# Kernel optimization log

Measured on AMD Instinct MI355X. Metric: run time of the kernel, lower is better.

The kernel has to match this reference:

```python
import jax, jax.numpy as jnp
import numpy as np
from jax import lax

B, C, T = 8, 512, 2048
TEMP = 0.07
EPS = 1e-12


def setup_inputs() -> dict:
    key = jax.random.key(0)
    k1, k2, k3, k4 = jax.random.split(key, 4)
    x = jax.random.normal(k1, (B, C, T), dtype=jnp.float32)
    w_qkv = jax.random.normal(k2, (3 * C, C, 1), dtype=jnp.float32) * (1.0 / np.sqrt(C))
    w_dw = jax.random.normal(k3, (3 * C, 1, 3), dtype=jnp.float32) * (1.0 / np.sqrt(3))
    w_proj = jax.random.normal(k4, (C, C, 1), dtype=jnp.float32) * (1.0 / np.sqrt(C))
    return {"x": x, "w_qkv": w_qkv, "w_dw": w_dw, "w_proj": w_proj}


def _l2norm_ch(a):
    # F.normalize(a, dim=1): divide by L2 norm over channel dim, clamped at eps
    n = jnp.sqrt(jnp.sum(a * a, axis=1, keepdims=True))
    return a / jnp.maximum(n, EPS)


def reference(x, w_qkv, w_dw, w_proj):
    # 1x1 conv: [B,C,T] x [3C,C] -> [B,3C,T]
    qkv = jnp.einsum('bct,oc->bot', x, w_qkv[:, :, 0])
    # depthwise conv, kernel 3, padding 1, groups = 3C
    qkv = lax.conv_general_dilated(
        qkv, w_dw, window_strides=(1,), padding=[(1, 1)],
        dimension_numbers=('NCH', 'OIH', 'NCH'), feature_group_count=3 * C)
    q, k, v = jnp.split(qkv, 3, axis=1)  # each [B,C,T]
    q = _l2norm_ch(q)
    k = _l2norm_ch(k)
    # attn over tokens: [B,T,T]
    attn = jax.nn.softmax(jnp.einsum('bct,bcs->bts', q, k) / TEMP, axis=-1)
    out = jnp.einsum('bts,bcs->bct', attn, v)  # [B,C,T]
    return jnp.einsum('bct,oc->bot', out, w_proj[:, :, 0])
```

## Files before the change

kernel.cpp:

```cpp
#include <hip/hip_runtime.h>
#include <math.h>

static constexpr int B_ = 8, C_ = 512, T_ = 2048, C3_ = 1536;
static constexpr float INV_TEMP = 1.0f / 0.07f;

typedef __attribute__((ext_vector_type(8))) short short8;
typedef __attribute__((ext_vector_type(4))) float floatx4;

__device__ __forceinline__ float b2f(unsigned short u) {
  union { unsigned int i; float f; } v; v.i = ((unsigned int)u) << 16; return v.f;
}
__device__ __forceinline__ unsigned short f2b(float f) {
  union { float f; unsigned int i; } v; v.f = f;
  const unsigned int x = v.i;
  return (unsigned short)((x + 0x7FFFu + ((x >> 16) & 1u)) >> 16);
}
__device__ __forceinline__ void gld16(const unsigned short* g, unsigned short* l) {
  __builtin_amdgcn_global_load_lds(
      (const __attribute__((address_space(1))) void*)g,
      (__attribute__((address_space(3))) void*)l, 16, 0, 0);
}

template<bool OUT_BF16, int MODE, int MAP = 0>
__global__ __launch_bounds__(256)
void gemm_tn(const unsigned short* __restrict__ A, const unsigned short* __restrict__ B,
             void* __restrict__ Cout, int K, int lda, int ldb, int ldc,
             long long sA, long long sB, long long sC,
             const float* __restrict__ rs, const float* __restrict__ cs,
             float* __restrict__ denom, int rcStride, float scale)
{
  constexpr int NL = 4;

  int bz, m0, n0;
  if (MAP == 2) {
    const int id = blockIdx.x;
    bz = id & 7;
    const int r = id >> 3;
    m0 = (r >> 2) * 128; n0 = (r & 3) * 128;
  } else {
    bz = blockIdx.z;
    m0 = blockIdx.y * 128; n0 = blockIdx.x * 128;
  }
  A += (long long)bz * sA;
  B += (long long)bz * sB;
  if (MODE == 2) { rs += (long long)bz * rcStride; cs += (long long)bz * rcStride;
                   denom += (long long)bz * rcStride; }
  if (MODE == 3) { rs += (long long)bz * rcStride; }
  const int tid = threadIdx.x;
  const int w = tid >> 6, lane = tid & 63;
  const int wm = (w >> 1) * 64, wn = (w & 1) * 64;
  const int rl = lane & 15, qd = lane >> 4;

  __shared__ __align__(16) unsigned short As[3][128 * 32];
  __shared__ __align__(16) unsigned short Bs[3][128 * 32];

  const int sr = lane >> 2, sg = lane & 3;
  const int ml0 = 32 * w + sr, ml1 = ml0 + 16;
  const int q0 = sg ^ ((ml0 >> 1) & 3), q1 = sg ^ ((ml1 >> 1) & 3);
  const unsigned short* gA0 = A + (long long)(m0 + ml0) * lda + q0 * 8;
  const unsigned short* gA1 = A + (long long)(m0 + ml1) * lda + q1 * 8;
  const unsigned short* gB0 = B + (long long)(n0 + ml0) * ldb + q0 * 8;
  const unsigned short* gB1 = B + (long long)(n0 + ml1) * ldb + q1 * 8;

  int aoff[4], boff[4];
  #pragma unroll
  for (int i = 0; i < 4; ++i) {
    const int mr = wm + i * 16 + rl;
    aoff[i] = mr * 32 + ((qd ^ ((mr >> 1) & 3)) * 8);
    const int nr = wn + i * 16 + rl;
    boff[i] = nr * 32 + ((qd ^ ((nr >> 1) & 3)) * 8);
  }

  floatx4 acc[4][4];
  #pragma unroll
  for (int i = 0; i < 4; ++i)
    #pragma unroll
    for (int j = 0; j < 4; ++j) acc[i][j] = 0.0f;

  auto stage = [&](int t, int bf) {
    const int ko = t * 32;
    gld16(gA0 + ko, As[bf] + (32 * w) * 32);
    gld16(gA1 + ko, As[bf] + (32 * w + 16) * 32);
    gld16(gB0 + ko, Bs[bf] + (32 * w) * 32);
    gld16(gB1 + ko, Bs[bf] + (32 * w + 16) * 32);
  };
  auto compute = [&](int bf) {
    short8 fa[4], fb[4];
    #pragma unroll
    for (int i = 0; i < 4; ++i) fa[i] = *(const short8*)(As[bf] + aoff[i]);
    #pragma unroll
    for (int j = 0; j < 4; ++j) fb[j] = *(const short8*)(Bs[bf] + boff[j]);
    #pragma unroll
    for (int i = 0; i < 4; ++i)
      #pragma unroll
      for (int j = 0; j < 4; ++j)
        acc[i][j] = __builtin_amdgcn_mfma_f32_16x16x32_bf16(fa[i], fb[j], acc[i][j], 0, 0, 0);
  };

  const int niter = K >> 5;
  stage(0, 0);
  stage(1, 1);
  int buf = 0;
  for (int i = 0; i < niter - 1; ++i) {
    asm volatile("s_waitcnt vmcnt(%0)\n\ts_barrier" :: "i"(NL) : "memory");
    if (i + 2 < niter) {
      int nb = buf + 2; if (nb >= 3) nb -= 3;
      stage(i + 2, nb);
    }
    compute(buf);
    if (++buf == 3) buf = 0;
  }
  asm volatile("s_waitcnt vmcnt(0)\n\ts_barrier" ::: "memory");
  compute(buf);

  #pragma unroll
  for (int i = 0; i < 4; ++i) {
    #pragma unroll
    for (int r = 0; r < 4; ++r) {
      const int row = m0 + wm + i * 16 + qd * 4 + r;
      float rowf = 0.f;
      if (MODE == 2) rowf = rs[row] * scale;
      if (MODE == 3) rowf = 1.0f / rs[row];
      float rsum = 0.f;
      #pragma unroll
      for (int j = 0; j < 4; ++j) {
        const int col = n0 + wn + j * 16 + rl;
        float v = acc[i][j][r];
        if (MODE == 2) {
          const float s = v * rowf * cs[col];
          const unsigned short pb = f2b(__expf(s - scale));
          rsum += b2f(pb);
          ((unsigned short*)Cout)[(long long)bz * sC + (long long)row * ldc + col] = pb;
          continue;
        }
        if (MODE == 3) v *= rowf;
        const long long idx = (long long)bz * sC + (long long)row * ldc + col;
        if (OUT_BF16) ((unsigned short*)Cout)[idx] = f2b(v);
        else          ((float*)Cout)[idx] = v;
      }
      if (MODE == 2) {
        #pragma unroll
        for (int m = 1; m < 16; m <<= 1) rsum += __shfl_xor(rsum, m);
        if (rl == 0) atomicAdd(denom + row, rsum);
      }
    }
  }
}

__global__ __launch_bounds__(512)
void gemm_attn8(const unsigned short* __restrict__ A, const unsigned short* __restrict__ B,
                unsigned short* __restrict__ Cout, int K, int lda, int ldb, int ldc,
                long long sA, long long sB, long long sC,
                const float* __restrict__ rs, const float* __restrict__ cs,
                float* __restrict__ denom, int rcStride, float scale)
{
  extern __shared__ unsigned short S[];

  const int id = blockIdx.x;
  const int bz = id & 7;
  const int r = id >> 3;
  const int m0 = (r >> 3) * 128, n0 = (r & 7) * 256;
  A += (long long)bz * sA;
  B += (long long)bz * sB;
  rs += (long long)bz * rcStride; cs += (long long)bz * rcStride;
  denom += (long long)bz * rcStride;
  const int tid = threadIdx.x;
  const int w = tid >> 6, lane = tid & 63;
  const int wm = (w >> 2) * 64, wn = (w & 3) * 64;
  const int rl = lane & 15, qd = lane >> 4;

  const int srw = tid >> 2, sg = tid & 3;
  const int qa  = sg ^ ((srw >> 1) & 3);
  const int brw1 = 128 + srw;
  const int qb1 = sg ^ ((brw1 >> 1) & 3);
  const unsigned short* gA  = A + (long long)(m0 + srw) * lda + qa * 8;
  const unsigned short* gB0 = B + (long long)(n0 + srw) * ldb + qa * 8;
  const unsigned short* gB1 = B + (long long)(n0 + brw1) * ldb + qb1 * 8;
  unsigned short* dA  = S + srw * 32 + sg * 8;
  unsigned short* dB0 = S + 12288 + srw * 32 + sg * 8;
  unsigned short* dB1 = S + 12288 + brw1 * 32 + sg * 8;

  int aoff[4], boff[4];
  #pragma unroll
  for (int i = 0; i < 4; ++i) {
    const int mr = wm + i * 16 + rl;
    aoff[i] = mr * 32 + ((qd ^ ((mr >> 1) & 3)) * 8);
    const int nr = wn + i * 16 + rl;
    boff[i] = 12288 + nr * 32 + ((qd ^ ((nr >> 1) & 3)) * 8);
  }

  floatx4 acc[4][4];
  #pragma unroll
  for (int i = 0; i < 4; ++i)
    #pragma unroll
    for (int j = 0; j < 4; ++j) acc[i][j] = 0.0f;

  auto stage = [&](int t, int bf) {
    const int ko = t * 32;
    gld16(gA + ko,  dA  + bf * 4096);
    gld16(gB0 + ko, dB0 + bf * 8192);
    gld16(gB1 + ko, dB1 + bf * 8192);
  };
  auto compute = [&](int bf) {
    short8 fa[4], fb[4];
    const unsigned short* pA = S + bf * 4096;
    const unsigned short* pB = S + bf * 8192;
    #pragma unroll
    for (int i = 0; i < 4; ++i) fa[i] = *(const short8*)(pA + aoff[i]);
    #pragma unroll
    for (int j = 0; j < 4; ++j) fb[j] = *(const short8*)(pB + boff[j]);
    #pragma unroll
    for (int i = 0; i < 4; ++i)
      #pragma unroll
      for (int j = 0; j < 4; ++j)
        acc[i][j] = __builtin_amdgcn_mfma_f32_16x16x32_bf16(fa[i], fb[j], acc[i][j], 0, 0, 0);
  };

  const int niter = K >> 5;
  stage(0, 0);
  stage(1, 1);
  int buf = 0;
  for (int i = 0; i < niter - 1; ++i) {
    asm volatile("s_waitcnt vmcnt(3)\n\ts_barrier" ::: "memory");
    if (i + 2 < niter) {
      int nb = buf + 2; if (nb >= 3) nb -= 3;
      stage(i + 2, nb);
    }
    compute(buf);
    if (++buf == 3) buf = 0;
  }
  asm volatile("s_waitcnt vmcnt(0)\n\ts_barrier" ::: "memory");
  compute(buf);

  float cf4[4];
  #pragma unroll
  for (int j = 0; j < 4; ++j) cf4[j] = cs[n0 + wn + j * 16 + rl];
  #pragma unroll
  for (int i = 0; i < 4; ++i) {
    #pragma unroll
    for (int rr = 0; rr < 4; ++rr) {
      const int row = m0 + wm + i * 16 + qd * 4 + rr;
      const float rowf = rs[row] * scale;
      float rsum = 0.f;
      #pragma unroll
      for (int j = 0; j < 4; ++j) {
        const int col = n0 + wn + j * 16 + rl;
        const float s = acc[i][j][rr] * rowf * cf4[j];
        const unsigned short pb = f2b(__expf(s - scale));
        rsum += b2f(pb);
        Cout[(long long)bz * sC + (long long)row * ldc + col] = pb;
      }
      #pragma unroll
      for (int m = 1; m < 16; m <<= 1) rsum += __shfl_xor(rsum, m);
      if (rl == 0) atomicAdd(denom + row, rsum);
    }
  }
}

__global__ __launch_bounds__(256)
void zero_f(float* __restrict__ p, int n)
{
  const int i = blockIdx.x * 256 + threadIdx.x;
  if (i < n) p[i] = 0.f;
}

__global__ __launch_bounds__(256)
void fin_inv(float* __restrict__ p, int n)
{
  const int i = blockIdx.x * 256 + threadIdx.x;
  if (i < n) p[i] = 1.f / fmaxf(sqrtf(p[i]), 1e-12f);
}

__global__ __launch_bounds__(256)
void conv_xT(const float* __restrict__ x, unsigned short* __restrict__ xT)
{
  const int b = blockIdx.z, t0 = blockIdx.x * 64, c0 = blockIdx.y * 64;
  const int tid = threadIdx.x;
  __shared__ float tile[64][65];
  const float* src = x + (long long)b * C_ * T_;
  const int cy = tid >> 2, g = tid & 3;
  const float* sp = src + (long long)(c0 + cy) * T_ + t0 + 16 * g;
  #pragma unroll
  for (int i = 0; i < 4; ++i) {
    const float4 v = *(const float4*)(sp + 4 * i);
    tile[cy][16 * g + 4 * i + 0] = v.x;
    tile[cy][16 * g + 4 * i + 1] = v.y;
    tile[cy][16 * g + 4 * i + 2] = v.z;
    tile[cy][16 * g + 4 * i + 3] = v.w;
  }
  __syncthreads();
  const int tl = tid >> 2, cg = tid & 3;
  short8 o0, o1;
  #pragma unroll
  for (int i = 0; i < 8; ++i) {
    o0[i] = (short)f2b(tile[16 * cg + i][tl]);
    o1[i] = (short)f2b(tile[16 * cg + 8 + i][tl]);
  }
  unsigned short* dst = xT + (long long)b * T_ * C_ + (long long)(t0 + tl) * C_ + c0 + 16 * cg;
  *(short8*)dst = o0;
  *(short8*)(dst + 8) = o1;
}

__global__ __launch_bounds__(256)
void conv_bf(const float* __restrict__ in, unsigned short* __restrict__ out, int n)
{
  const int i = blockIdx.x * 256 + threadIdx.x;
  if (i < n) out[i] = f2b(in[i]);
}

__global__ __launch_bounds__(256)
void dw_qkv_v2(const unsigned short* __restrict__ qkv, const float* __restrict__ wdw,
               unsigned short* __restrict__ qT, unsigned short* __restrict__ kT,
               unsigned short* __restrict__ vout,
               float* __restrict__ sq_q, float* __restrict__ sq_k)
{
  const int bz = blockIdx.z, b = bz / 3, p = bz % 3;
  const int t0 = blockIdx.x * 64, c0 = blockIdx.y * 64;
  const int tid = threadIdx.x;
  __shared__ unsigned short tin[64][80];
  __shared__ float tout[64][65];
  const int chb = b * C3_ + p * C_;

  #pragma unroll
  for (int s = 0; s < 2; ++s) {
    const int idx = tid + s * 256;
    const int cy = idx >> 3, g = idx & 7;
    *(short8*)&tin[cy][8 + 8 * g] =
        *(const short8*)(qkv + (long long)(chb + c0 + cy) * T_ + t0 + 8 * g);
  }
  if (tid < 64) {
    tin[tid][7] = (t0 > 0) ? qkv[(long long)(chb + c0 + tid) * T_ + t0 - 1]
                           : (unsigned short)0;
  } else if (tid < 128) {
    const int cy = tid - 64;
    tin[cy][72] = (t0 + 64 < T_) ? qkv[(long long)(chb + c0 + cy) * T_ + t0 + 64]
                                 : (unsigned short)0;
  }
  __syncthreads();

  const int cy = tid >> 2, tg = tid & 3;
  const float* wp = wdw + (p * C_ + c0 + cy) * 3;
  const float w0 = wp[0], w1 = wp[1], w2 = wp[2];

  if (p == 2) {
    short8 o0, o1;
    #pragma unroll
    for (int i = 0; i < 16; ++i) {
      const int j = 16 * tg + i;
      const float v = fmaf(w0, b2f(tin[cy][7 + j]),
                      fmaf(w1, b2f(tin[cy][8 + j]), w2 * b2f(tin[cy][9 + j])));
      if (i < 8) o0[i] = (short)f2b(v); else o1[i - 8] = (short)f2b(v);
    }
    unsigned short* d = vout + (long long)(b * C_ + c0 + cy) * T_ + t0 + 16 * tg;
    *(short8*)d = o0;
    *(short8*)(d + 8) = o1;
    return;
  }

  #pragma unroll
  for (int i = 0; i < 16; ++i) {
    const int j = 16 * tg + i;
    tout[j][cy] = fmaf(w0, b2f(tin[cy][7 + j]),
                  fmaf(w1, b2f(tin[cy][8 + j]), w2 * b2f(tin[cy][9 + j])));
  }
  __syncthreads();

  unsigned short* dst = (p == 0 ? qT : kT) + (long long)b * T_ * C_;
  float* sq = (p == 0 ? sq_q : sq_k) + (long long)b * T_;
  #pragma unroll
  for (int s = 0; s < 2; ++s) {
    const int idx = tid + s * 256;
    const int tl = idx >> 3, cl = idx & 7;
    short8 o;
    float ssq = 0.f;
    #pragma unroll
    for (int i = 0; i < 8; ++i) {
      const unsigned short ub = f2b(tout[tl][8 * cl + i]);
      o[i] = (short)ub;
      const float fv = b2f(ub);
      ssq = fmaf(fv, fv, ssq);
    }
    *(short8*)(dst + (long long)(t0 + tl) * C_ + c0 + 8 * cl) = o;
    #pragma unroll
    for (int m = 1; m < 8; m <<= 1) ssq += __shfl_xor(ssq, m);
    if (cl == 0) atomicAdd(sq + t0 + tl, ssq);
  }
}

extern "C" void kernel_launch(void* const* d_in, const int* in_sizes, int n_in,
                              void* d_out, int out_size, void* d_ws, size_t ws_size,
                              hipStream_t stream)
{
  const float* x      = (const float*)d_in[0];
  const float* w_qkv  = (const float*)d_in[1];
  const float* w_dw   = (const float*)d_in[2];
  const float* w_proj = (const float*)d_in[3];
  float* out = (float*)d_out;

  static int attr_done = 0;
  if (!attr_done) {
    hipFuncSetAttribute((const void*)&gemm_attn8,
                        hipFuncAttributeMaxDynamicSharedMemorySize, 73728);
    attr_done = 1;
  }

  char* base = (char*)d_ws;
  unsigned short* xT      = (unsigned short*)base;
  unsigned short* wqkv_bf = (unsigned short*)(base + 16777216);
  unsigned short* av_t    = (unsigned short*)base;
  char* p = base + 67108864;
  unsigned short* qT = (unsigned short*)p; p += 16777216;
  unsigned short* kT = (unsigned short*)p; p += 16777216;
  unsigned short* vb = (unsigned short*)p; p += 16777216;
  unsigned short* attn   = (unsigned short*)p;
  unsigned short* qkv_bf = (unsigned short*)p;
  p += 67108864;
  unsigned short* wproj_bf = (unsigned short*)p; p += 524288;
  float* inv_nq = (float*)p; p += 65536;
  float* inv_nk = (float*)p; p += 65536;
  float* denom  = (float*)p;

  const long long TC = (long long)T_ * C_, TT = (long long)T_ * T_;

  conv_xT<<<dim3(T_ / 64, C_ / 64, B_), 256, 0, stream>>>(x, xT);
  conv_bf<<<(C3_ * C_) / 256, 256, 0, stream>>>(w_qkv, wqkv_bf, C3_ * C_);
  conv_bf<<<(C_ * C_) / 256, 256, 0, stream>>>(w_proj, wproj_bf, C_ * C_);
  zero_f<<<(3 * B_ * T_) / 256, 256, 0, stream>>>(inv_nq, 3 * B_ * T_);

  gemm_tn<true, 0><<<dim3(16, 12, B_), 256, 0, stream>>>(
      wqkv_bf, xT, qkv_bf, C_, C_, C_, T_,
      0LL, TC, (long long)C3_ * T_, nullptr, nullptr, nullptr, 0, 1.f);

  dw_qkv_v2<<<dim3(T_ / 64, C_ / 64, B_ * 3), 256, 0, stream>>>(
      qkv_bf, w_dw, qT, kT, vb, inv_nq, inv_nk);
  fin_inv<<<(2 * B_ * T_) / 256, 256, 0, stream>>>(inv_nq, 2 * B_ * T_);

  gemm_attn8<<<dim3(128 * B_, 1, 1), 512, 73728, stream>>>(
      qT, kT, attn, C_, C_, C_, T_,
      TC, TC, TT, inv_nq, inv_nk, denom, T_, INV_TEMP);

  gemm_tn<true, 3, 2><<<dim3(64 * B_, 1, 1), 256, 0, stream>>>(
      attn, vb, av_t, T_, T_, T_, C_,
      TT, (long long)C_ * T_, TC, denom, nullptr, nullptr, T_, 1.f);

  gemm_tn<false, 0><<<dim3(16, 4, B_), 256, 0, stream>>>(
      wproj_bf, av_t, out, C_, C_, C_, T_,
      0LL, TC, (long long)C_ * T_, nullptr, nullptr, nullptr, 0, 1.f);
}
```

Before: 275.8 us.

## Enlarge QK^T attention GEMM tile to 256x256 with 4x8 MFMA per-wave tiles

The attention score GEMM now uses 256x256 output tiles instead of 128x256. Each of the 8 waves computes a 64x128 sub-tile with a 4x8 accumulator array, and the global-to-LDS staging is reorganised into four 16-byte loads per thread. Grid size is halved, and LDS per block grows to 96 KB across three buffers. The aim is more reuse per LDS fragment load and less global traffic for A and B, at the cost of higher register pressure (128 accumulator floats per thread) and fewer blocks to fill the CUs.

```diff
diff --git a/kernel.cpp b/kernel.cpp
--- a/kernel.cpp
+++ b/kernel.cpp
@@ -147,72 +147,73 @@
   }
 }
 
-__global__ __launch_bounds__(512)
-void gemm_attn8(const unsigned short* __restrict__ A, const unsigned short* __restrict__ B,
-                unsigned short* __restrict__ Cout, int K, int lda, int ldb, int ldc,
-                long long sA, long long sB, long long sC,
-                const float* __restrict__ rs, const float* __restrict__ cs,
-                float* __restrict__ denom, int rcStride, float scale)
+__global__ __launch_bounds__(512, 2)
+void gemm_attn512(const unsigned short* __restrict__ A, const unsigned short* __restrict__ B,
+                  unsigned short* __restrict__ Cout, int K, int lda, int ldb, int ldc,
+                  long long sA, long long sB, long long sC,
+                  const float* __restrict__ rs, const float* __restrict__ cs,
+                  float* __restrict__ denom, int rcStride, float scale)
 {
   extern __shared__ unsigned short S[];
 
   const int id = blockIdx.x;
   const int bz = id & 7;
   const int r = id >> 3;
-  const int m0 = (r >> 3) * 128, n0 = (r & 7) * 256;
+  const int m0 = (r >> 3) * 256, n0 = (r & 7) * 256;
   A += (long long)bz * sA;
   B += (long long)bz * sB;
   rs += (long long)bz * rcStride; cs += (long long)bz * rcStride;
   denom += (long long)bz * rcStride;
+
   const int tid = threadIdx.x;
   const int w = tid >> 6, lane = tid & 63;
-  const int wm = (w >> 2) * 64, wn = (w & 3) * 64;
+  const int wm = (w >> 1) * 64, wn = (w & 1) * 128;
   const int rl = lane & 15, qd = lane >> 4;
 
-  const int srw = tid >> 2, sg = tid & 3;
-  const int qa  = sg ^ ((srw >> 1) & 3);
-  const int brw1 = 128 + srw;
-  const int qb1 = sg ^ ((brw1 >> 1) & 3);
-  const unsigned short* gA  = A + (long long)(m0 + srw) * lda + qa * 8;
-  const unsigned short* gB0 = B + (long long)(n0 + srw) * ldb + qa * 8;
-  const unsigned short* gB1 = B + (long long)(n0 + brw1) * ldb + qb1 * 8;
-  unsigned short* dA  = S + srw * 32 + sg * 8;
-  unsigned short* dB0 = S + 12288 + srw * 32 + sg * 8;
-  unsigned short* dB1 = S + 12288 + brw1 * 32 + sg * 8;
-
-  int aoff[4], boff[4];
+  const int srow = w * 16 + (lane >> 2), sg = lane & 3;
+  const int qa = sg ^ ((srow >> 1) & 3);
+  const unsigned short* gA0 = A + (long long)(m0 + srow) * lda + qa * 8;
+  const unsigned short* gA1 = gA0 + (long long)128 * lda;
+  const unsigned short* gB0 = B + (long long)(n0 + srow) * ldb + qa * 8;
+  const unsigned short* gB1 = gB0 + (long long)128 * ldb;
+
+  int aoff[4], boff[8];
   #pragma unroll
   for (int i = 0; i < 4; ++i) {
-    const int mr = wm + i * 16 + rl;
-    aoff[i] = mr * 32 + ((qd ^ ((mr >> 1) & 3)) * 8);
-    const int nr = wn + i * 16 + rl;
-    boff[i] = 12288 + nr * 32 + ((qd ^ ((nr >> 1) & 3)) * 8);
-  }
-
-  floatx4 acc[4][4];
+    const int ar = wm + i * 16 + rl;
+    aoff[i] = ar * 32 + ((qd ^ ((ar >> 1) & 3)) * 8);
+  }
+  #pragma unroll
+  for (int j = 0; j < 8; ++j) {
+    const int br = wn + j * 16 + rl;
+    boff[j] = 8192 + br * 32 + ((qd ^ ((br >> 1) & 3)) * 8);
+  }
+
+  floatx4 acc[4][8];
   #pragma unroll
   for (int i = 0; i < 4; ++i)
     #pragma unroll
-    for (int j = 0; j < 4; ++j) acc[i][j] = 0.0f;
+    for (int j = 0; j < 8; ++j) acc[i][j] = 0.0f;
 
   auto stage = [&](int t, int bf) {
     const int ko = t * 32;
-    gld16(gA + ko,  dA  + bf * 4096);
-    gld16(gB0 + ko, dB0 + bf * 8192);
-    gld16(gB1 + ko, dB1 + bf * 8192);
+    unsigned short* base = S + bf * 16384;
+    gld16(gA0 + ko, base + w * 512);
+    gld16(gA1 + ko, base + 4096 + w * 512);
+    gld16(gB0 + ko, base + 8192 + w * 512);
+    gld16(gB1 + ko, base + 12288 + w * 512);
   };
   auto compute = [&](int bf) {
-    short8 fa[4], fb[4];
-    const unsigned short* pA = S + bf * 4096;
-    const unsigned short* pB = S + bf * 8192;
-    #pragma unroll
-    for (int i = 0; i < 4; ++i) fa[i] = *(const short8*)(pA + aoff[i]);
-    #pragma unroll
-    for (int j = 0; j < 4; ++j) fb[j] = *(const short8*)(pB + boff[j]);
+    short8 fa[4], fb[8];
+    const unsigned short* base = S + bf * 16384;
+    #pragma unroll
+    for (int i = 0; i < 4; ++i) fa[i] = *(const short8*)(base + aoff[i]);
+    #pragma unroll
+    for (int j = 0; j < 8; ++j) fb[j] = *(const short8*)(base + boff[j]);
     #pragma unroll
     for (int i = 0; i < 4; ++i)
       #pragma unroll
-      for (int j = 0; j < 4; ++j)
+      for (int j = 0; j < 8; ++j)
         acc[i][j] = __builtin_amdgcn_mfma_f32_16x16x32_bf16(fa[i], fb[j], acc[i][j], 0, 0, 0);
   };
 
@@ -221,7 +222,7 @@
   stage(1, 1);
   int buf = 0;
   for (int i = 0; i < niter - 1; ++i) {
-    asm volatile("s_waitcnt vmcnt(3)\n\ts_barrier" ::: "memory");
+    asm volatile("s_waitcnt vmcnt(4)\n\ts_barrier" ::: "memory");
     if (i + 2 < niter) {
       int nb = buf + 2; if (nb >= 3) nb -= 3;
       stage(i + 2, nb);
@@ -232,9 +233,9 @@
   asm volatile("s_waitcnt vmcnt(0)\n\ts_barrier" ::: "memory");
   compute(buf);
 
-  float cf4[4];
-  #pragma unroll
-  for (int j = 0; j < 4; ++j) cf4[j] = cs[n0 + wn + j * 16 + rl];
+  float cf[8];
+  #pragma unroll
+  for (int j = 0; j < 8; ++j) cf[j] = cs[n0 + wn + j * 16 + rl];
   #pragma unroll
   for (int i = 0; i < 4; ++i) {
     #pragma unroll
@@ -243,9 +244,9 @@
       const float rowf = rs[row] * scale;
       float rsum = 0.f;
       #pragma unroll
-      for (int j = 0; j < 4; ++j) {
+      for (int j = 0; j < 8; ++j) {
         const int col = n0 + wn + j * 16 + rl;
-        const float s = acc[i][j][rr] * rowf * cf4[j];
+        const float s = acc[i][j][rr] * rowf * cf[j];
         const unsigned short pb = f2b(__expf(s - scale));
         rsum += b2f(pb);
         Cout[(long long)bz * sC + (long long)row * ldc + col] = pb;
@@ -399,8 +400,8 @@
 
   static int attr_done = 0;
   if (!attr_done) {
-    hipFuncSetAttribute((const void*)&gemm_attn8,
-                        hipFuncAttributeMaxDynamicSharedMemorySize, 73728);
+    hipFuncSetAttribute((const void*)&gemm_attn512,
+                        hipFuncAttributeMaxDynamicSharedMemorySize, 98304);
     attr_done = 1;
   }
 
@@ -435,7 +436,7 @@
       qkv_bf, w_dw, qT, kT, vb, inv_nq, inv_nk);
   fin_inv<<<(2 * B_ * T_) / 256, 256, 0, stream>>>(inv_nq, 2 * B_ * T_);
 
-  gemm_attn8<<<dim3(128 * B_, 1, 1), 512, 73728, stream>>>(
+  gemm_attn512<<<dim3(64 * B_, 1, 1), 512, 98304, stream>>>(
       qT, kT, attn, C_, C_, C_, T_,
       TC, TC, TT, inv_nq, inv_nk, denom, T_, INV_TEMP);
 
```

New measurement: 282.4 us. 1.02x slower.
